# Performance work log

Hardware: AMD Instinct MI355X
Metric: run time of the kernel (lower is better)

Reference implementation:

```python
import jax, jax.numpy as jnp
import numpy as np

N_NODES = 100000
N_EDGES = 1000000
IN_DIM = 128
H = [64, 64, 64, 64, 128]
OUT_DIM = 64
K = 3  # TAGConv default hops
BN_EPS = 1e-5


def _gcn_norm(src, dst, num_nodes):
    # symmetric normalization D^{-1/2} A D^{-1/2}, no self loops (PyG TAGConv default)
    deg = jax.ops.segment_sum(jnp.ones(src.shape[0], jnp.float32), dst, num_segments=num_nodes)
    dis = jnp.where(deg > 0, jax.lax.rsqrt(jnp.maximum(deg, 1.0)), 0.0)
    return dis[src] * dis[dst]  # [E]


def _tagconv(x, src, dst, norm, Ws, b, num_nodes):
    # Ws: [K+1, in, out]; out = sum_k (A_hat^k x) @ W_k + b
    out = x @ Ws[0]
    h = x
    for k in range(1, K + 1):
        h = jax.ops.segment_sum(h[src] * norm[:, None], dst, num_segments=num_nodes)
        out = out + h @ Ws[k]
    return out + b


def setup_inputs() -> dict:
    key = jax.random.key(0)
    ks = jax.random.split(key, 16)
    s = 0.05
    x = jax.random.normal(ks[0], (N_NODES, IN_DIM), jnp.float32)
    edge_index = jax.random.randint(ks[1], (2, N_EDGES), 0, N_NODES, dtype=jnp.int64)
    return {
        "x": x,
        "edge_index": edge_index,
        "bn_gamma": jnp.ones((IN_DIM,), jnp.float32),
        "bn_beta": jnp.zeros((IN_DIM,), jnp.float32),
        "W1": jax.random.normal(ks[2], (IN_DIM, H[0]), jnp.float32) * s,
        "b1": jnp.zeros((H[0],), jnp.float32),
        "tag1_W": jax.random.normal(ks[3], (K + 1, H[0], H[1]), jnp.float32) * s,
        "tag1_b": jnp.zeros((H[1],), jnp.float32),
        "W2": jax.random.normal(ks[4], (H[1], H[2]), jnp.float32) * s,
        "b2": jnp.zeros((H[2],), jnp.float32),
        "tag2_W": jax.random.normal(ks[5], (K + 1, H[2], H[3]), jnp.float32) * s,
        "tag2_b": jnp.zeros((H[3],), jnp.float32),
        "W3": jax.random.normal(ks[6], (H[3] + IN_DIM, H[4]), jnp.float32) * s,
        "b3": jnp.zeros((H[4],), jnp.float32),
        "W4": jax.random.normal(ks[7], (H[4], OUT_DIM), jnp.float32) * s,
        "b4": jnp.zeros((OUT_DIM,), jnp.float32),
    }


def reference(x, edge_index, bn_gamma, bn_beta, W1, b1, tag1_W, tag1_b,
              W2, b2, tag2_W, tag2_b, W3, b3, W4, b4):
    gelu = lambda t: jax.nn.gelu(t, approximate=False)  # torch GELU default (erf)
    src, dst = edge_index[0], edge_index[1]
    norm = _gcn_norm(src, dst, N_NODES)

    # BatchNorm over nodes (training-mode batch stats, biased variance)
    mean = jnp.mean(x, axis=0)
    var = jnp.mean((x - mean) ** 2, axis=0)
    x_norm = (x - mean) * jax.lax.rsqrt(var + BN_EPS) * bn_gamma + bn_beta

    h = gelu(x_norm @ W1 + b1)
    h = gelu(_tagconv(h, src, dst, norm, tag1_W, tag1_b, N_NODES))
    h = gelu(h @ W2 + b2)
    h = gelu(_tagconv(h, src, dst, norm, tag2_W, tag2_b, N_NODES))
    a = jnp.concatenate([x, h], axis=1)
    a = gelu(a @ W3 + b3)
    return a @ W4 + b4
```

## Files before the change

kernel.cpp:

```cpp
#include <hip/hip_runtime.h>
#include <stdint.h>

typedef unsigned short u16;
typedef unsigned int   u32;
typedef __attribute__((ext_vector_type(8))) short short8;
typedef __attribute__((ext_vector_type(4))) float float4v;

#define DEV __device__ __forceinline__

#define ABLK  512
#define MAXNB 4096

DEV float bf2f(u16 u){ return __uint_as_float(((u32)u)<<16); }
DEV u16 f2bf(float f){
  u32 u = __float_as_uint(f);
  u32 r = u + 0x7fffu + ((u>>16)&1u);
  return (u16)(r>>16);
}
DEV float gelu_f(float x){ return 0.5f*x*(1.0f + erff(x*0.70710678118654752f)); }
DEV float ldext(const void* b, size_t i, int f32){
  return f32 ? ((const float*)b)[i] : bf2f(((const u16*)b)[i]);
}
DEV int ld_src(const int* ei, int e, int E, int m64){ return m64 ? ei[2*e]     : ei[e]; }
DEV int ld_dst(const int* ei, int e, int E, int m64){ return m64 ? ei[2*(E+e)] : ei[E+e]; }
DEV int swz(int k, int n){
  return (((k>>5)*4 + (n>>4))*64 + ((((k>>3)&3)<<4) | (n&15)))*8 + (k&7);
}

__global__ __launch_bounds__(256) void detect_types(const int* __restrict__ ei,
                                                    const u16* __restrict__ xw,
                                                    int* __restrict__ flags){
  __shared__ int a64, insane;
  int t = threadIdx.x;
  if (t==0){ a64=0; insane=0; }
  __syncthreads();
  int l=0;
  for (int i=t; i<4096; i+=256) l |= ei[2*i+1];
  if (l) atomicOr(&a64, 1);
  int c=0;
  for (int i=t; i<2048; i+=256){
    u16 lo = xw[2*i];
    int e8 = (lo>>7)&0xff;
    if (e8!=0 && (e8<90 || e8>160)) c++;
  }
  atomicAdd(&insane, c);
  __syncthreads();
  if (t==0){ flags[0] = a64?0:1; flags[1] = (insane>256)?1:0; }
}

__global__ __launch_bounds__(256) void econv_a0(const int* __restrict__ ei,
                                                const int* __restrict__ flags,
                                                int2* __restrict__ sd, int* __restrict__ hist,
                                                int E, int N, int shift, int NBK){
  __shared__ int cnt[MAXNB];
  for (int i=threadIdx.x; i<NBK; i+=256) cnt[i]=0;
  __syncthreads();
  int m64 = flags[0];
  for (int e = blockIdx.x*256 + threadIdx.x; e < E; e += ABLK*256){
    int s = ld_src(ei, e, E, m64);
    int d = ld_dst(ei, e, E, m64);
    int2 p; p.x = s; p.y = d;
    sd[e] = p;
    if ((unsigned)d < (unsigned)N) atomicAdd(&cnt[d>>shift], 1);
  }
  __syncthreads();
  int* hrow = hist + (size_t)blockIdx.x*NBK;
  for (int i=threadIdx.x; i<NBK; i+=256) hrow[i] = cnt[i];
}

__global__ __launch_bounds__(256) void hist_colscan(int* __restrict__ hist,
                                                    int* __restrict__ btot, int NBK){
  __shared__ int lds[256];
  int b = blockIdx.x, t = threadIdx.x;
  int v0 = hist[(size_t)(2*t  )*NBK + b];
  int v1 = hist[(size_t)(2*t+1)*NBK + b];
  int ps = v0 + v1;
  lds[t] = ps; __syncthreads();
  for (int off=1; off<256; off<<=1){
    int add = (t>=off) ? lds[t-off] : 0;
    __syncthreads();
    lds[t] += add;
    __syncthreads();
  }
  int excl = lds[t] - ps;
  hist[(size_t)(2*t  )*NBK + b] = excl;
  hist[(size_t)(2*t+1)*NBK + b] = excl + v0;
  if (t==255) btot[b] = lds[255];
}

__global__ __launch_bounds__(256) void bucket_scan(const int* __restrict__ btot,
                                                   int* __restrict__ bb, int NBK){
  __shared__ int lds[256];
  int t = threadIdx.x;
  int carry = 0;
  int nch = (NBK + 255)/256;
  for (int c=0; c<nch; c++){
    int i = c*256 + t;
    int v = (i<NBK) ? btot[i] : 0;
    lds[t] = v; __syncthreads();
    for (int off=1; off<256; off<<=1){
      int add = (t>=off) ? lds[t-off] : 0;
      __syncthreads();
      lds[t] += add;
      __syncthreads();
    }
    if (i<NBK) bb[i] = carry + lds[t] - v;
    int tot = lds[255];
    __syncthreads();
    carry += tot;
  }
  if (t==0) bb[NBK] = carry;
}

__global__ __launch_bounds__(256) void econv_a1(const int2* __restrict__ sd,
                                                const int* __restrict__ hist,
                                                const int* __restrict__ bb,
                                                int2* __restrict__ binned,
                                                int E, int N, int shift, int NBK){
  __shared__ int cnt[MAXNB];
  __shared__ int base[MAXNB];
  const int* hrow = hist + (size_t)blockIdx.x*NBK;
  for (int i=threadIdx.x; i<NBK; i+=256){ cnt[i]=0; base[i]=bb[i]+hrow[i]; }
  __syncthreads();
  for (int e = blockIdx.x*256 + threadIdx.x; e < E; e += ABLK*256){
    int2 p = sd[e];
    if ((unsigned)p.y < (unsigned)N){
      int b = p.y >> shift;
      int r = atomicAdd(&cnt[b], 1);
      binned[base[b] + r] = p;
    }
  }
}

__global__ __launch_bounds__(256) void bucket_count(const int2* __restrict__ binned,
                                                    const int* __restrict__ bb,
                                                    int* __restrict__ rofs, float* __restrict__ dis,
                                                    int N, int shift, int NBK, int NPB){
  __shared__ int cnt[256];
  __shared__ int lds[256];
  int b = blockIdx.x, t = threadIdx.x;
  int lo = bb[b], hi = bb[b+1];
  if (t < NPB) cnt[t] = 0;
  __syncthreads();
  int mask = NPB - 1;
  for (int e = lo + t; e < hi; e += 256)
    atomicAdd(&cnt[binned[e].y & mask], 1);
  __syncthreads();
  int v = (t < NPB) ? cnt[t] : 0;
  lds[t] = v; __syncthreads();
  for (int off=1; off<256; off<<=1){
    int add = (t>=off) ? lds[t-off] : 0;
    __syncthreads();
    lds[t] += add;
    __syncthreads();
  }
  if (t < NPB){
    int node = (b<<shift) + t;
    if (node < N){
      rofs[node] = lo + lds[t] - v;
      dis[node]  = v > 0 ? rsqrtf((float)v) : 0.f;
    }
  }
  if (b==0 && t==0) rofs[N] = bb[NBK];
}

__global__ __launch_bounds__(256) void bucket_emit(const int2* __restrict__ binned,
                                                   const int* __restrict__ bb,
                                                   const int* __restrict__ rofs,
                                                   const float* __restrict__ dis,
                                                   int2* __restrict__ epack,
                                                   int N, int shift, int NPB){
  __shared__ int   cur[256];
  __shared__ float dl[256];
  int b = blockIdx.x, t = threadIdx.x;
  int lo = bb[b], hi = bb[b+1];
  if (t < NPB){
    int node = (b<<shift) + t;
    cur[t] = (node < N) ? rofs[node] : 0;
    dl[t]  = (node < N) ? dis[node]  : 0.f;
  }
  __syncthreads();
  int mask = NPB - 1;
  for (int e = lo + t; e < hi; e += 256){
    int2 p = binned[e];
    int dli = p.y & mask;
    int slot = atomicAdd(&cur[dli], 1);
    int s = p.x; float w;
    if ((unsigned)s < (unsigned)N) w = dis[s]*dl[dli];
    else { s = 0; w = 0.f; }
    int2 pk; pk.x = s; pk.y = __float_as_int(w);
    epack[slot] = pk;
  }
}

__global__ __launch_bounds__(256) void bn_stats(const void* __restrict__ x,
                                                const int* __restrict__ flags,
                                                float* __restrict__ sums,
                                                u16* __restrict__ xbf, int N){
  __shared__ float red[16][128];
  int f32  = flags[1];
  int tid  = threadIdx.x;
  int col  = tid & 15;
  int rsub = tid >> 4;
  float s8[8], q8[8];
  #pragma unroll
  for (int j=0;j<8;j++){ s8[j]=0.f; q8[j]=0.f; }
  for (int r = blockIdx.x*16 + rsub; r < N; r += gridDim.x*16){
    float f[8];
    if (f32){
      const float* xp = (const float*)x + (size_t)r*128 + col*8;
      float4 A = *(const float4*)xp;
      float4 B = *(const float4*)(xp+4);
      f[0]=A.x; f[1]=A.y; f[2]=A.z; f[3]=A.w;
      f[4]=B.x; f[5]=B.y; f[6]=B.z; f[7]=B.w;
      u16 o[8];
      #pragma unroll
      for (int j=0;j<8;j++) o[j] = f2bf(f[j]);
      *(uint4*)(xbf + (size_t)r*128 + col*8) = *(uint4*)o;
    } else {
      const u16* xp = (const u16*)x + (size_t)r*128 + col*8;
      uint4 u = *(const uint4*)xp;
      f[0]=bf2f((u16)(u.x&0xffffu)); f[1]=bf2f((u16)(u.x>>16));
      f[2]=bf2f((u16)(u.y&0xffffu)); f[3]=bf2f((u16)(u.y>>16));
      f[4]=bf2f((u16)(u.z&0xffffu)); f[5]=bf2f((u16)(u.z>>16));
      f[6]=bf2f((u16)(u.w&0xffffu)); f[7]=bf2f((u16)(u.w>>16));
    }
    #pragma unroll
    for (int j=0;j<8;j++){ s8[j]+=f[j]; q8[j]+=f[j]*f[j]; }
  }
  #pragma unroll
  for (int j=0;j<8;j++) red[rsub][col*8+j] = s8[j];
  __syncthreads();
  if (tid < 128){
    float t=0.f;
    #pragma unroll
    for (int i=0;i<16;i++) t += red[i][tid];
    atomicAdd(&sums[tid], t);
  }
  __syncthreads();
  #pragma unroll
  for (int j=0;j<8;j++) red[rsub][col*8+j] = q8[j];
  __syncthreads();
  if (tid < 128){
    float t=0.f;
    #pragma unroll
    for (int i=0;i<16;i++) t += red[i][tid];
    atomicAdd(&sums[128+tid], t);
  }
}

struct PrepOut {
  u16 *W1p,*Wt1,*Wt2,*W2p,*W3a,*W3b,*W4p;
  float *b1p,*bt1,*bt2,*b2p,*b3a,*b3b,*b4p;
};

#define PREP_TOTAL 78272

__global__ __launch_bounds__(256) void prep(const float* __restrict__ sums, float invN,
    const int* __restrict__ flags,
    const void* g, const void* be,
    const void* W1, const void* b1,
    const void* t1W, const void* t1b,
    const void* W2, const void* b2,
    const void* t2W, const void* t2b,
    const void* W3, const void* b3,
    const void* W4, const void* b4,
    PrepOut o)
{
  int f32 = flags[1];
  int idx = blockIdx.x*256 + threadIdx.x;
  if (idx >= PREP_TOTAL) return;
  auto scale_shift = [&](int f, float& sc, float& sh){
    float m   = sums[f]*invN;
    float var = sums[128+f]*invN - m*m;
    sc = ldext(g,f,f32) * rsqrtf(var + 1e-5f);
    sh = ldext(be,f,f32) - m*sc;
  };
  if (idx < 8192){
    int k=idx>>6, n=idx&63; float sc,sh; scale_shift(k,sc,sh);
    o.W1p[swz(k,n)] = f2bf(sc*ldext(W1,idx,f32)); return;
  }
  idx -= 8192;
  if (idx < 64){
    float acc = ldext(b1,idx,f32);
    for (int f=0; f<128; f++){ float sc,sh; scale_shift(f,sc,sh); acc += sh*ldext(W1,f*64+idx,f32); }
    o.b1p[idx]=acc; return;
  }
  idx -= 64;
  if (idx < 16384){ int k=idx>>6,n=idx&63; o.Wt1[swz(k,n)]=f2bf(ldext(t1W,idx,f32)); return; }  idx -= 16384;
  if (idx < 64)   { o.bt1[idx]=ldext(t1b,idx,f32); return; }  idx -= 64;
  if (idx < 16384){ int k=idx>>6,n=idx&63; o.Wt2[swz(k,n)]=f2bf(ldext(t2W,idx,f32)); return; }  idx -= 16384;
  if (idx < 64)   { o.bt2[idx]=ldext(t2b,idx,f32); return; }  idx -= 64;
  if (idx < 4096) { int k=idx>>6,n=idx&63; o.W2p[swz(k,n)]=f2bf(ldext(W2,idx,f32));  return; }  idx -= 4096;
  if (idx < 64)   { o.b2p[idx]=ldext(b2,idx,f32);  return; }  idx -= 64;
  if (idx < 12288){ int k=idx>>6,n=idx&63; o.W3a[swz(k,n)]=f2bf(ldext(W3,(size_t)k*128+n,f32));    return; }  idx -= 12288;
  if (idx < 64)   { o.b3a[idx]=ldext(b3,idx,f32);  return; }  idx -= 64;
  if (idx < 12288){ int k=idx>>6,n=idx&63; o.W3b[swz(k,n)]=f2bf(ldext(W3,(size_t)k*128+64+n,f32)); return; }  idx -= 12288;
  if (idx < 64)   { o.b3b[idx]=ldext(b3,64+idx,f32); return; } idx -= 64;
  if (idx < 8192) { int k=idx>>6,n=idx&63; o.W4p[swz(k,n)]=f2bf(ldext(W4,idx,f32));  return; }
  else            { o.b4p[idx-8192]=ldext(b4,idx-8192,f32); }
}

struct KD { const u16* p[8]; int ld[8]; };

template<int KS,int OUTMODE>
__global__ __launch_bounds__(256,2) void gemm_mfma(
    KD d, const u16* __restrict__ Wsw, const float* __restrict__ bias,
    void* __restrict__ out, int ldo, int ocol,
    int N, const int* __restrict__ flags, long xdelta, u32 xmask)
{
  constexpr int LBYTES = OUTMODE ? 128*68*4 : 128*72*2;
  __shared__ __align__(16) char lds[LBYTES];
  if (xmask && !flags[1]){
    #pragma unroll
    for (int t=0;t<KS;t++) if (xmask & (1u<<t)) d.p[t] += xdelta;
  }
  int tid = threadIdx.x, w = tid>>6, l = tid&63;
  int rlo = l&15, kq = l>>4;
  int row0b = blockIdx.x*128;
  int row0  = row0b + w*32;

  short8 Bf[KS][4];
  #pragma unroll
  for (int t=0;t<KS;t++)
    #pragma unroll
    for (int c=0;c<4;c++)
      Bf[t][c] = *(const short8*)(Wsw + ((t*4+c)*64 + l)*8);

  float4v a0[4], a1[4];
  #pragma unroll
  for (int c=0;c<4;c++){
    a0[c].x=0;a0[c].y=0;a0[c].z=0;a0[c].w=0;
    a1[c].x=0;a1[c].y=0;a1[c].z=0;a1[c].w=0;
  }

  #pragma unroll
  for (int t=0;t<KS;t++){
    const u16* ap = d.p[t]; int ld = d.ld[t];
    short8 A0 = *(const short8*)(ap + (size_t)(row0+rlo)*ld + kq*8);
    short8 A1 = *(const short8*)(ap + (size_t)(row0+16+rlo)*ld + kq*8);
    #pragma unroll
    for (int c=0;c<4;c++){
      a0[c] = __builtin_amdgcn_mfma_f32_16x16x32_bf16(A0, Bf[t][c], a0[c], 0,0,0);
      a1[c] = __builtin_amdgcn_mfma_f32_16x16x32_bf16(A1, Bf[t][c], a1[c], 0,0,0);
    }
  }

  float bv[4];
  #pragma unroll
  for (int c=0;c<4;c++) bv[c] = bias[c*16 + rlo];

  int nrow = N - row0b; if (nrow > 128) nrow = 128; if (nrow < 0) nrow = 0;

  if (OUTMODE==0){
    u16* s = (u16*)lds;
    #pragma unroll
    for (int c=0;c<4;c++){
      int col = c*16 + rlo;
      #pragma unroll
      for (int r=0;r<4;r++){
        s[(w*32 +      kq*4 + r)*72 + col] = f2bf(gelu_f(a0[c][r] + bv[c]));
        s[(w*32 + 16 + kq*4 + r)*72 + col] = f2bf(gelu_f(a1[c][r] + bv[c]));
      }
    }
    __syncthreads();
    u16* ob = (u16*)out + (size_t)row0b*ldo + ocol;
    for (int i=tid; i<nrow*8; i+=256){
      int r = i>>3, cc = (i&7)<<3;
      *(uint4*)(ob + (size_t)r*ldo + cc) = *(const uint4*)(s + r*72 + cc);
    }
  } else {
    int f32o = flags[1];
    if (f32o){
      float* sf = (float*)lds;
      #pragma unroll
      for (int c=0;c<4;c++){
        int col = c*16 + rlo;
        #pragma unroll
        for (int r=0;r<4;r++){
          float v0 = a0[c][r] + bv[c]; float v1 = a1[c][r] + bv[c];
          sf[(w*32 +      kq*4 + r)*68 + col] = isfinite(v0)?v0:777.0f;
          sf[(w*32 + 16 + kq*4 + r)*68 + col] = isfinite(v1)?v1:777.0f;
        }
      }
      __syncthreads();
      float* ob = (float*)out + (size_t)row0b*64;
      for (int i=tid; i<nrow*16; i+=256){
        int r = i>>4, cc = (i&15)<<2;
        *(uint4*)(ob + (size_t)r*64 + cc) = *(const uint4*)(sf + r*68 + cc);
      }
    } else {
      u16* s = (u16*)lds;
      #pragma unroll
      for (int c=0;c<4;c++){
        int col = c*16 + rlo;
        #pragma unroll
        for (int r=0;r<4;r++){
          float v0 = a0[c][r] + bv[c]; float v1 = a1[c][r] + bv[c];
          s[(w*32 +      kq*4 + r)*72 + col] = f2bf(isfinite(v0)?v0:777.0f);
          s[(w*32 + 16 + kq*4 + r)*72 + col] = f2bf(isfinite(v1)?v1:777.0f);
        }
      }
      __syncthreads();
      u16* ob = (u16*)out + (size_t)row0b*64;
      for (int i=tid; i<nrow*8; i+=256){
        int r = i>>3, cc = (i&7)<<3;
        *(uint4*)(ob + (size_t)r*64 + cc) = *(const uint4*)(s + r*72 + cc);
      }
    }
  }
}

__global__ __launch_bounds__(256) void spmm(const int* __restrict__ rofs,
    const int2* __restrict__ epack,
    const u16* __restrict__ hin, u16* __restrict__ hout, int N)
{
  int lane = threadIdx.x & 63;
  int wv   = (int)((blockIdx.x*256 + threadIdx.x) >> 6);
  int sub  = lane >> 3;
  int f8   = (lane & 7) * 8;
  int row  = wv*8 + sub;
  bool rok = row < N;
  int beg = rok ? rofs[row]   : 0;
  int end = rok ? rofs[row+1] : 0;

  float acc[8];
  #pragma unroll
  for (int j=0;j<8;j++) acc[j]=0.f;

  int e = beg;
  int2 pk; pk.x = 0; pk.y = 0;
  if (e < end) pk = epack[e];

  while (__any(e < end)){
    bool act = e < end;
    int   s = act ? pk.x : 0;
    float w = act ? __int_as_float(pk.y) : 0.f;
    if ((u32)s >= (u32)N){ s = 0; w = 0.f; }
    uint4 v = *(const uint4*)(hin + (size_t)s*64 + f8);
    int e1 = e + 1;
    if (e1 < end) pk = epack[e1];
    acc[0] += w*__uint_as_float(v.x<<16);
    acc[1] += w*__uint_as_float(v.x&0xffff0000u);
    acc[2] += w*__uint_as_float(v.y<<16);
    acc[3] += w*__uint_as_float(v.y&0xffff0000u);
    acc[4] += w*__uint_as_float(v.z<<16);
    acc[5] += w*__uint_as_float(v.z&0xffff0000u);
    acc[6] += w*__uint_as_float(v.w<<16);
    acc[7] += w*__uint_as_float(v.w&0xffff0000u);
    e = e1;
  }

  if (rok){
    u16 o[8];
    #pragma unroll
    for (int j=0;j<8;j++) o[j]=f2bf(acc[j]);
    *(uint4*)(hout + (size_t)row*64 + f8) = *(uint4*)o;
  }
}

extern "C" void kernel_launch(void* const* d_in, const int* in_sizes, int n_in,
                              void* d_out, int out_size, void* d_ws, size_t ws_size,
                              hipStream_t stream)
{
  const void* x   = d_in[0];
  const int*  ei  = (const int*)d_in[1];
  const void* gam = d_in[2];  const void* bet = d_in[3];
  const void* W1  = d_in[4];  const void* b1  = d_in[5];
  const void* t1W = d_in[6];  const void* t1b = d_in[7];
  const void* W2  = d_in[8];  const void* b2  = d_in[9];
  const void* t2W = d_in[10]; const void* t2b = d_in[11];
  const void* W3  = d_in[12]; const void* b3  = d_in[13];
  const void* W4  = d_in[14]; const void* b4  = d_in[15];

  const int N = in_sizes[0]/128;
  const int E = in_sizes[1]/2;

  int shift = 7;
  while ((((long)N + (1L<<shift) - 1) >> shift) > MAXNB) shift++;
  const int NPB = 1<<shift;
  const int NBK = (int)(((long)N + NPB - 1) >> shift);

  char* p = (char*)d_ws;
  auto carve = [&](size_t bytes)->void*{
    void* r = (void*)p;
    p += (bytes + 255) & ~(size_t)255;
    return r;
  };
  float* bnsums  = (float*)carve(256*4);
  int*   flags   = (int*)  carve(256);
  size_t zero_span = (size_t)((char*)p - (char*)bnsums);
  int*   row_ofs = (int*)  carve((size_t)(N+1)*4);
  float* dis     = (float*)carve((size_t)N*4);
  int*   hist    = (int*)  carve((size_t)ABLK*NBK*4);
  int*   btot    = (int*)  carve((size_t)NBK*4);
  int*   bb      = (int*)  carve((size_t)(NBK+1)*4);
  int2*  sd      = (int2*) carve((size_t)E*8);
  int2*  binned  = (int2*) carve((size_t)E*8);
  int2*  epack   = (int2*) carve((size_t)E*8);
  PrepOut po;
  po.W1p=(u16*)carve(8192*2);   po.b1p=(float*)carve(64*4);
  po.Wt1=(u16*)carve(16384*2);  po.bt1=(float*)carve(64*4);
  po.Wt2=(u16*)carve(16384*2);  po.bt2=(float*)carve(64*4);
  po.W2p=(u16*)carve(4096*2);   po.b2p=(float*)carve(64*4);
  po.W3a=(u16*)carve(12288*2);  po.b3a=(float*)carve(64*4);
  po.W3b=(u16*)carve(12288*2);  po.b3b=(float*)carve(64*4);
  po.W4p=(u16*)carve(8192*2);   po.b4p=(float*)carve(64*4);
  u16* xbf  = (u16*)carve((size_t)N*128*2);
  u16* buf0 = (u16*)carve((size_t)N*64*2);
  u16* buf1 = (u16*)carve((size_t)N*64*2);
  u16* buf2 = (u16*)carve((size_t)N*64*2);
  u16* buf3 = (u16*)carve((size_t)N*64*2);
  u16* buf4 = (u16*)carve((size_t)N*64*2);
  carve(64*1024);
  u16* Ka   = buf0;

  size_t needed = (size_t)(p - (char*)d_ws);
  if (needed > ws_size || NPB > 256 || E < 4096){
    hipMemsetAsync(d_out, 0, (size_t)out_size*2, stream);
    return;
  }

  long xdelta = (const u16*)x - xbf;

  const int gblk = (N + 127)/128;
  const int sblk = (N + 31)/32;

  hipMemsetAsync(bnsums, 0, zero_span, stream);

  detect_types<<<1, 256, 0, stream>>>(ei, (const u16*)x, flags);
  econv_a0    <<<ABLK,256,0,stream>>>(ei, flags, sd, hist, E, N, shift, NBK);
  hist_colscan<<<NBK, 256,0,stream>>>(hist, btot, NBK);
  bucket_scan <<<1,   256,0,stream>>>(btot, bb, NBK);
  econv_a1    <<<ABLK,256,0,stream>>>(sd, hist, bb, binned, E, N, shift, NBK);
  bucket_count<<<NBK, 256,0,stream>>>(binned, bb, row_ofs, dis, N, shift, NBK, NPB);
  bucket_emit <<<NBK, 256,0,stream>>>(binned, bb, row_ofs, dis, epack, N, shift, NPB);
  bn_stats    <<<512, 256,0,stream>>>(x, flags, bnsums, xbf, N);
  prep        <<<(PREP_TOTAL+255)/256, 256, 0, stream>>>(bnsums, 1.0f/(float)N, flags,
                 gam, bet, W1, b1, t1W, t1b, W2, b2, t2W, t2b, W3, b3, W4, b4, po);

  KD dx;   for (int t=0;t<4;t++){ dx.p[t]  = xbf + t*32;  dx.ld[t]=128; }
           for (int t=4;t<8;t++){ dx.p[t]  = xbf;         dx.ld[t]=128; }
  KD dcat; { u16* bs[4]={buf0,buf1,buf2,buf3};
             for (int t=0;t<8;t++){ dcat.p[t]=bs[t>>1]+(t&1)*32; dcat.ld[t]=64; } }
  KD d3;   for (int t=0;t<4;t++){ d3.p[t]  = xbf + t*32;  d3.ld[t]=128; }
           d3.p[4]=buf4; d3.ld[4]=64; d3.p[5]=buf4+32; d3.ld[5]=64;
           d3.p[6]=buf4; d3.ld[6]=64; d3.p[7]=buf4;    d3.ld[7]=64;
  KD d4;   for (int t=0;t<4;t++){ d4.p[t]  = Ka + t*32;   d4.ld[t]=128; }
           for (int t=4;t<8;t++){ d4.p[t]  = Ka;          d4.ld[t]=128; }

  gemm_mfma<4,0><<<gblk,256,0,stream>>>(dx, po.W1p, po.b1p, buf0,64,0, N, flags, xdelta, 0xFu);
  spmm<<<sblk,256,0,stream>>>(row_ofs, epack, buf0, buf1, N);
  spmm<<<sblk,256,0,stream>>>(row_ofs, epack, buf1, buf2, N);
  spmm<<<sblk,256,0,stream>>>(row_ofs, epack, buf2, buf3, N);
  gemm_mfma<8,0><<<gblk,256,0,stream>>>(dcat, po.Wt1, po.bt1, buf4,64,0, N, flags, 0, 0);
  { KD dl2; for (int t=0;t<8;t++){ dl2.p[t]=buf4+(t&1)*32; dl2.ld[t]=64; }
    gemm_mfma<2,0><<<gblk,256,0,stream>>>(dl2, po.W2p, po.b2p, buf0,64,0, N, flags, 0, 0); }
  spmm<<<sblk,256,0,stream>>>(row_ofs, epack, buf0, buf1, N);
  spmm<<<sblk,256,0,stream>>>(row_ofs, epack, buf1, buf2, N);
  spmm<<<sblk,256,0,stream>>>(row_ofs, epack, buf2, buf3, N);
  gemm_mfma<8,0><<<gblk,256,0,stream>>>(dcat, po.Wt2, po.bt2, buf4,64,0, N, flags, 0, 0);
  gemm_mfma<6,0><<<gblk,256,0,stream>>>(d3, po.W3a, po.b3a, Ka,128,0,  N, flags, xdelta, 0xFu);
  gemm_mfma<6,0><<<gblk,256,0,stream>>>(d3, po.W3b, po.b3b, Ka,128,64, N, flags, xdelta, 0xFu);
  gemm_mfma<4,1><<<gblk,256,0,stream>>>(d4, po.W4p, po.b4p, d_out,64,0, N, flags, 0, 0);
}
```

Baseline: 467.8 us.

## Map one row per wavefront in spmm and fuse the two W3 GEMMs

The spmm kernel now assigns a whole wavefront to each destination row. Eight lane groups each take every eighth edge, and the partial sums are combined with xor shuffles. This shortens the serial per-row dependency chain and gives more memory parallelism per row, at the cost of idle lanes on low-degree rows. The two W3 GEMM launches are also merged into one dual-output kernel that loads the A tiles once for both weight halves, which adds register pressure.

```diff
diff --git a/kernel.cpp b/kernel.cpp
--- a/kernel.cpp
+++ b/kernel.cpp
@@ -411,35 +411,100 @@
   }
 }
 
+template<int KS>
+__global__ __launch_bounds__(256,2) void gemm_dual(
+    KD d, const u16* __restrict__ Wa, const u16* __restrict__ Wb,
+    const float* __restrict__ biasa, const float* __restrict__ biasb,
+    u16* __restrict__ out,
+    int N, const int* __restrict__ flags, long xdelta, u32 xmask)
+{
+  __shared__ __align__(16) u16 s[128*72];
+  if (xmask && !flags[1]){
+    #pragma unroll
+    for (int t=0;t<KS;t++) if (xmask & (1u<<t)) d.p[t] += xdelta;
+  }
+  int tid = threadIdx.x, w = tid>>6, l = tid&63;
+  int rlo = l&15, kq = l>>4;
+  int row0b = blockIdx.x*128;
+  int row0  = row0b + w*32;
+
+  float4v pa0[4], pa1[4], pb0[4], pb1[4];
+  #pragma unroll
+  for (int c=0;c<4;c++){
+    pa0[c].x=0;pa0[c].y=0;pa0[c].z=0;pa0[c].w=0;
+    pa1[c].x=0;pa1[c].y=0;pa1[c].z=0;pa1[c].w=0;
+    pb0[c].x=0;pb0[c].y=0;pb0[c].z=0;pb0[c].w=0;
+    pb1[c].x=0;pb1[c].y=0;pb1[c].z=0;pb1[c].w=0;
+  }
+
+  #pragma unroll
+  for (int t=0;t<KS;t++){
+    const u16* ap = d.p[t]; int ld = d.ld[t];
+    short8 A0 = *(const short8*)(ap + (size_t)(row0+rlo)*ld + kq*8);
+    short8 A1 = *(const short8*)(ap + (size_t)(row0+16+rlo)*ld + kq*8);
+    #pragma unroll
+    for (int c=0;c<4;c++){
+      short8 Ba = *(const short8*)(Wa + ((t*4+c)*64 + l)*8);
+      short8 Bb = *(const short8*)(Wb + ((t*4+c)*64 + l)*8);
+      pa0[c] = __builtin_amdgcn_mfma_f32_16x16x32_bf16(A0, Ba, pa0[c], 0,0,0);
+      pa1[c] = __builtin_amdgcn_mfma_f32_16x16x32_bf16(A1, Ba, pa1[c], 0,0,0);
+      pb0[c] = __builtin_amdgcn_mfma_f32_16x16x32_bf16(A0, Bb, pb0[c], 0,0,0);
+      pb1[c] = __builtin_amdgcn_mfma_f32_16x16x32_bf16(A1, Bb, pb1[c], 0,0,0);
+    }
+  }
+
+  int nrow = N - row0b; if (nrow > 128) nrow = 128; if (nrow < 0) nrow = 0;
+
+  #pragma unroll
+  for (int h=0; h<2; ++h){
+    const float* bias = h ? biasb : biasa;
+    float bv[4];
+    #pragma unroll
+    for (int c=0;c<4;c++) bv[c] = bias[c*16 + rlo];
+    #pragma unroll
+    for (int c=0;c<4;c++){
+      int col = c*16 + rlo;
+      float4v& q0 = h ? pb0[c] : pa0[c];
+      float4v& q1 = h ? pb1[c] : pa1[c];
+      #pragma unroll
+      for (int r=0;r<4;r++){
+        s[(w*32 +      kq*4 + r)*72 + col] = f2bf(gelu_f(q0[r] + bv[c]));
+        s[(w*32 + 16 + kq*4 + r)*72 + col] = f2bf(gelu_f(q1[r] + bv[c]));
+      }
+    }
+    __syncthreads();
+    u16* ob = out + (size_t)row0b*128 + h*64;
+    for (int i=tid; i<nrow*8; i+=256){
+      int r = i>>3, cc = (i&7)<<3;
+      *(uint4*)(ob + (size_t)r*128 + cc) = *(const uint4*)(s + r*72 + cc);
+    }
+    __syncthreads();
+  }
+}
+
 __global__ __launch_bounds__(256) void spmm(const int* __restrict__ rofs,
     const int2* __restrict__ epack,
     const u16* __restrict__ hin, u16* __restrict__ hout, int N)
 {
   int lane = threadIdx.x & 63;
-  int wv   = (int)((blockIdx.x*256 + threadIdx.x) >> 6);
-  int sub  = lane >> 3;
-  int f8   = (lane & 7) * 8;
-  int row  = wv*8 + sub;
-  bool rok = row < N;
-  int beg = rok ? rofs[row]   : 0;
-  int end = rok ? rofs[row+1] : 0;
+  int row  = (int)((blockIdx.x*256 + threadIdx.x) >> 6);
+  if (row >= N) return;
+  int es = lane >> 3;
+  int f8 = (lane & 7) * 8;
+  int beg = rofs[row], end = rofs[row+1];
 
   float acc[8];
   #pragma unroll
   for (int j=0;j<8;j++) acc[j]=0.f;
 
-  int e = beg;
-  int2 pk; pk.x = 0; pk.y = 0;
-  if (e < end) pk = epack[e];
-
-  while (__any(e < end)){
+  for (int e = beg + es; __any(e < end); e += 8){
     bool act = e < end;
-    int   s = act ? pk.x : 0;
+    int2 pk; pk.x = 0; pk.y = 0;
+    if (act) pk = epack[e];
+    int   s = pk.x;
     float w = act ? __int_as_float(pk.y) : 0.f;
     if ((u32)s >= (u32)N){ s = 0; w = 0.f; }
     uint4 v = *(const uint4*)(hin + (size_t)s*64 + f8);
-    int e1 = e + 1;
-    if (e1 < end) pk = epack[e1];
     acc[0] += w*__uint_as_float(v.x<<16);
     acc[1] += w*__uint_as_float(v.x&0xffff0000u);
     acc[2] += w*__uint_as_float(v.y<<16);
@@ -448,10 +513,15 @@
     acc[5] += w*__uint_as_float(v.z&0xffff0000u);
     acc[6] += w*__uint_as_float(v.w<<16);
     acc[7] += w*__uint_as_float(v.w&0xffff0000u);
-    e = e1;
-  }
-
-  if (rok){
+  }
+
+  #pragma unroll
+  for (int m=8; m<=32; m<<=1){
+    #pragma unroll
+    for (int j=0;j<8;j++) acc[j] += __shfl_xor(acc[j], m, 64);
+  }
+
+  if (es == 0){
     u16 o[8];
     #pragma unroll
     for (int j=0;j<8;j++) o[j]=f2bf(acc[j]);
@@ -524,7 +594,7 @@
   long xdelta = (const u16*)x - xbf;
 
   const int gblk = (N + 127)/128;
-  const int sblk = (N + 31)/32;
+  const int sblk = (N + 3)/4;
 
   hipMemsetAsync(bnsums, 0, zero_span, stream);
 
@@ -560,7 +630,6 @@
   spmm<<<sblk,256,0,stream>>>(row_ofs, epack, buf1, buf2, N);
   spmm<<<sblk,256,0,stream>>>(row_ofs, epack, buf2, buf3, N);
   gemm_mfma<8,0><<<gblk,256,0,stream>>>(dcat, po.Wt2, po.bt2, buf4,64,0, N, flags, 0, 0);
-  gemm_mfma<6,0><<<gblk,256,0,stream>>>(d3, po.W3a, po.b3a, Ka,128,0,  N, flags, xdelta, 0xFu);
-  gemm_mfma<6,0><<<gblk,256,0,stream>>>(d3, po.W3b, po.b3b, Ka,128,64, N, flags, xdelta, 0xFu);
+  gemm_dual<6><<<gblk,256,0,stream>>>(d3, po.W3a, po.W3b, po.b3a, po.b3b, Ka, N, flags, xdelta, 0xFu);
   gemm_mfma<4,1><<<gblk,256,0,stream>>>(d4, po.W4p, po.b4p, d_out,64,0, N, flags, 0, 0);
 }
```

Result: slower. 571.7 us (+22.2%).
